# Kernel optimization log

Measured on AMD Instinct MI355X. Metric: run time of the kernel, lower is better.

The kernel has to match this reference:

```python
import jax, jax.numpy as jnp
import numpy as np

L = 3          # layers
D = 256        # hidden_dim
H = 4          # heads
F = 1024       # ffn_size
IMG = (64, 32) # img_dim
S = IMG[0] * IMG[1]
DK = D // H    # key/query head dim
V = 2 * D      # double_v_dim value dim
DV = V // H    # value head dim
B = 2


def _rel_pos():
    # rotary angles, repeated pairwise as in get_rel_pos
    angle = 1.0 / (10000.0 ** jnp.linspace(0.0, 1.0, DK // 2))
    angle = jnp.repeat(angle, 2)                                  # [DK]
    idx = jnp.arange(S, dtype=jnp.float32)
    sin = jnp.sin(idx[:, None] * angle[None, :])                  # [S, DK]
    cos = jnp.cos(idx[:, None] * angle[None, :])
    # per-head causal decay mask, row-normalized by sqrt(rowsum)
    decay = jnp.log(1.0 - 2.0 ** (-5.0 - jnp.arange(H, dtype=jnp.float32)))  # [H]
    diff = idx[:, None] - idx[None, :]                            # [S, S]
    mask = jnp.where(diff >= 0, jnp.exp(diff[None, :, :] * decay[:, None, None]), 0.0)
    mask = mask / jnp.sqrt(mask.sum(-1, keepdims=True))           # [H, S, S]
    return sin, cos, mask


def _theta_shift(x, sin, cos):
    # x: [B, H, S, DK]; rotate-every-two rotary embedding
    x1, x2 = x[..., ::2], x[..., 1::2]
    rot = jnp.stack([-x2, x1], axis=-1).reshape(x.shape)
    return x * cos + rot * sin


def _ln(x, w, b, eps=1e-5):
    mu = x.mean(-1, keepdims=True)
    var = ((x - mu) ** 2).mean(-1, keepdims=True)
    return (x - mu) / jnp.sqrt(var + eps) * w + b


def _retention(x, sin, cos, mask, Wq, Wk, Wv, Wg, Wo):
    b, s, _ = x.shape
    q = (x @ Wq).reshape(b, s, H, DK).transpose(0, 2, 1, 3)
    k = (x @ Wk).reshape(b, s, H, DK).transpose(0, 2, 1, 3) * (DK ** -0.5)
    v = (x @ Wv).reshape(b, s, H, DV).transpose(0, 2, 1, 3)
    g = x @ Wg                                                    # [b, s, V]
    qr = _theta_shift(q, sin, cos)
    kr = _theta_shift(k, sin, cos)
    qk = jnp.einsum('bhsd,bhtd->bhst', qr, kr) * mask[None]
    denom = jnp.clip(jnp.abs(qk).sum(-1, keepdims=True), 1.0, None)
    qk = qk / jax.lax.stop_gradient(denom)
    o = jnp.einsum('bhst,bhtv->bhsv', qk, v)                      # [b, H, s, DV]
    o = o * jax.lax.rsqrt((o ** 2).mean(-1, keepdims=True) + 1e-6)  # per-head RMSNorm
    o = o.transpose(0, 2, 1, 3).reshape(b, s, V)
    o = (g * jax.nn.sigmoid(g)) * o                               # swish gate
    return o @ Wo


def setup_inputs():
    key = jax.random.key(0)
    ks = jax.random.split(key, 16)
    sc = 0.02
    return {
        'x': jax.random.normal(ks[0], (B, S, D), jnp.float32),
        'Wq': jax.random.normal(ks[1], (L, D, D), jnp.float32) * sc,
        'Wk': jax.random.normal(ks[2], (L, D, D), jnp.float32) * sc,
        'Wv': jax.random.normal(ks[3], (L, D, V), jnp.float32) * sc,
        'Wg': jax.random.normal(ks[4], (L, D, V), jnp.float32) * sc,
        'Wo': jax.random.normal(ks[5], (L, V, D), jnp.float32) * sc,
        'ln1_w': jnp.ones((L, D), jnp.float32),
        'ln1_b': jnp.zeros((L, D), jnp.float32),
        'ln2_w': jnp.ones((L, D), jnp.float32),
        'ln2_b': jnp.zeros((L, D), jnp.float32),
        'W1': jax.random.normal(ks[6], (L, D, F), jnp.float32) * sc,
        'b1': jnp.zeros((L, F), jnp.float32),
        'W2': jax.random.normal(ks[7], (L, F, D), jnp.float32) * sc,
        'b2': jnp.zeros((L, D), jnp.float32),
    }


def reference(x, Wq, Wk, Wv, Wg, Wo, ln1_w, ln1_b, ln2_w, ln2_b, W1, b1, W2, b2):
    sin, cos, mask = _rel_pos()
    for i in range(L):
        y = _retention(_ln(x, ln1_w[i], ln1_b[i]), sin, cos, mask,
                       Wq[i], Wk[i], Wv[i], Wg[i], Wo[i]) + x
        h = _ln(y, ln2_w[i], ln2_b[i])
        x = (jax.nn.gelu(h @ W1[i] + b1[i], approximate=False) @ W2[i] + b2[i]) + y
    return x.reshape(x.shape[0], IMG[0], IMG[1], D)
```

## Files before the change

kernel.cpp:

```cpp
#include <hip/hip_runtime.h>
#include <hip/hip_bf16.h>
#include <cstddef>
#include <cmath>
#include <algorithm>

#define SEQ 2048
#define DMODEL 256
#define NHEAD 4
#define DK 64
#define VDIM 512
#define DV 128
#define NB 2
#define FDIM 1024
#define NROWS (NB*SEQ)
#define QKVGN 1536
#define NSLOT 288

typedef unsigned short u16;
typedef __attribute__((ext_vector_type(8))) short short8;
typedef __attribute__((ext_vector_type(4))) short short4v;
typedef __attribute__((ext_vector_type(4))) float f32x4;

static __device__ __forceinline__ u16 f2b(float f) {
    union { float f; unsigned u; } c; c.f = f;
    unsigned r = c.u + 0x7fffu + ((c.u >> 16) & 1u);
    return (u16)(r >> 16);
}
static __device__ __forceinline__ float b2f(u16 u) {
    union { unsigned u; float f; } c; c.u = ((unsigned)u) << 16; return c.f;
}

static __device__ __forceinline__ f32x4 mfma16_bf16(short4v a, short4v b, f32x4 c) {
    return __builtin_amdgcn_mfma_f32_16x16x16bf16_1k(a, b, c, 0, 0, 0);
}

static __device__ __forceinline__ short4v pack_bf16x4(float a0, float a1, float a2, float a3) {
    union { short4v v; unsigned u[2]; } z;
    union { __hip_bfloat162 h; unsigned u; } p0, p1;
    p0.h = __float22bfloat162_rn(make_float2(a0, a1));
    p1.h = __float22bfloat162_rn(make_float2(a2, a3));
    z.u[0] = p0.u; z.u[1] = p1.u;
    return z.v;
}

#define GLOAD_LDS16(GP, LP) \
    __builtin_amdgcn_global_load_lds((const __attribute__((address_space(1))) void*)(GP), \
                                     (__attribute__((address_space(3))) void*)(LP), 16, 0, 0)

__global__ void tables_kernel(float* __restrict__ sint, float* __restrict__ cost)
{
    int idx = blockIdx.x * 256 + threadIdx.x;
    if (idx >= SEQ * DK) return;
    int s = idx >> 6, d = idx & 63;
    int j = d >> 1;
    float a = powf(10000.f, -(float)j / 31.f);
    float arg = (float)s * a;
    sint[idx] = sinf(arg);
    cost[idx] = cosf(arg);
}

__global__ __launch_bounds__(256) void wconv_kernel(const float* __restrict__ in,
                                                    u16* __restrict__ out, int K, int N,
                                                    size_t in_lstride, size_t out_lstride)
{
    __shared__ float tile[32][33];
    int n0 = blockIdx.x * 32, k0 = blockIdx.y * 32;
    const float* inz = in + (size_t)blockIdx.z * in_lstride;
    u16* outz = out + (size_t)blockIdx.z * out_lstride;
    int tx = threadIdx.x, ty = threadIdx.y;
    #pragma unroll
    for (int r = 0; r < 4; ++r) {
        int kr = ty + r * 8;
        tile[kr][tx] = inz[(size_t)(k0 + kr) * N + n0 + tx];
    }
    __syncthreads();
    #pragma unroll
    for (int r = 0; r < 4; ++r) {
        int nr = ty + r * 8;
        outz[(size_t)(n0 + nr) * K + k0 + tx] = f2b(tile[tx][nr]);
    }
}

__global__ __launch_bounds__(256) void ln_kernel(const float* __restrict__ x,
                                                 const float* __restrict__ w,
                                                 const float* __restrict__ b,
                                                 u16* __restrict__ o)
{
    int row = blockIdx.x;
    int t = threadIdx.x;
    float v = x[(size_t)row * DMODEL + t];
    __shared__ float red[256];
    red[t] = v; __syncthreads();
    for (int st = 128; st > 0; st >>= 1) { if (t < st) red[t] += red[t + st]; __syncthreads(); }
    float mu = red[0] * (1.f / DMODEL);
    __syncthreads();
    red[t] = v * v; __syncthreads();
    for (int st = 128; st > 0; st >>= 1) { if (t < st) red[t] += red[t + st]; __syncthreads(); }
    float var = red[0] * (1.f / DMODEL) - mu * mu;
    o[(size_t)row * DMODEL + t] = f2b((v - mu) * rsqrtf(var + 1e-5f) * w[t] + b[t]);
}

template<int NPART, int HASBIAS>
__global__ __launch_bounds__(256) void lncomb_kernel(const u16* __restrict__ pW,
                                                     const float* __restrict__ bias,
                                                     const float* __restrict__ res,
                                                     const float* __restrict__ w,
                                                     const float* __restrict__ b,
                                                     float* __restrict__ yout,
                                                     u16* __restrict__ o)
{
    int row = blockIdx.x;
    int t = threadIdx.x;
    size_t i = (size_t)row * DMODEL + t;
    const size_t PS = (size_t)NROWS * DMODEL;
    float v = res[i];
    #pragma unroll
    for (int k = 0; k < NPART; ++k) v += b2f(pW[i + k * PS]);
    if (HASBIAS) v += bias[t];
    yout[i] = v;
    __shared__ float red[256];
    red[t] = v; __syncthreads();
    for (int st = 128; st > 0; st >>= 1) { if (t < st) red[t] += red[t + st]; __syncthreads(); }
    float mu = red[0] * (1.f / DMODEL);
    __syncthreads();
    red[t] = v * v; __syncthreads();
    for (int st = 128; st > 0; st >>= 1) { if (t < st) red[t] += red[t + st]; __syncthreads(); }
    float var = red[0] * (1.f / DMODEL) - mu * mu;
    o[i] = f2b((v - mu) * rsqrtf(var + 1e-5f) * w[t] + b[t]);
}

__global__ __launch_bounds__(256) void comb4_kernel(const u16* __restrict__ pW,
                                                    const float* __restrict__ bias,
                                                    const float* __restrict__ yb,
                                                    float* __restrict__ out)
{
    int row = blockIdx.x;
    int t = threadIdx.x;
    size_t i = (size_t)row * DMODEL + t;
    const size_t PS = (size_t)NROWS * DMODEL;
    out[i] = b2f(pW[i]) + b2f(pW[i + PS]) + b2f(pW[i + 2 * PS]) + b2f(pW[i + 3 * PS]) + bias[t] + yb[i];
}

template<int BIAS, int GELU, int ROT, int OUTBF, int SPLIT, int VT>
__global__ __launch_bounds__(256) void gemm64(const u16* __restrict__ A,
                                              const u16* __restrict__ Bt,
                                              void* __restrict__ Cout,
                                              const float* __restrict__ bias,
                                              const float* __restrict__ sint,
                                              const float* __restrict__ cost,
                                              u16* __restrict__ vtout,
                                              int M, int N, int K, int kslice)
{
    __shared__ __align__(16) u16 As[2][64 * 64];
    __shared__ __align__(16) u16 Bs[2][64 * 64];
    int bx = blockIdx.x, by = blockIdx.y;
    int tid = threadIdx.x;
    int wave = tid >> 6, lane = tid & 63;
    int wm = wave & 1, wn = wave >> 1;
    int l15 = lane & 15, lg = lane >> 4;
    int kb0 = SPLIT ? blockIdx.z * kslice : 0;
    int kcnt = SPLIT ? kslice : K;

    int L0 = wave * 64 + lane;
    int r0 = L0 >> 3, c0g = (L0 & 7) ^ ((r0 >> 1) & 7);
    int L1 = 256 + wave * 64 + lane;
    int r1 = L1 >> 3, c1g = (L1 & 7) ^ ((r1 >> 1) & 7);
    const u16* Ag0 = A + (size_t)(by * 64 + r0) * K + kb0 + c0g * 8;
    const u16* Ag1 = A + (size_t)(by * 64 + r1) * K + kb0 + c1g * 8;
    const u16* Bg0 = Bt + (size_t)(bx * 64 + r0) * K + kb0 + c0g * 8;
    const u16* Bg1 = Bt + (size_t)(bx * 64 + r1) * K + kb0 + c1g * 8;

#define GSTAGE(BUF, KOFF) do { \
    GLOAD_LDS16(Ag0 + (KOFF), &As[BUF][wave * 512]); \
    GLOAD_LDS16(Ag1 + (KOFF), &As[BUF][2048 + wave * 512]); \
    GLOAD_LDS16(Bg0 + (KOFF), &Bs[BUF][wave * 512]); \
    GLOAD_LDS16(Bg1 + (KOFF), &Bs[BUF][2048 + wave * 512]); \
} while (0)

    f32x4 acc[2][2] = {};
    GSTAGE(0, 0);
    __syncthreads();
    int cur = 0;
    for (int k0 = 0; k0 < kcnt; k0 += 64, cur ^= 1) {
        if (k0 + 64 < kcnt) GSTAGE(cur ^ 1, k0 + 64);
        #pragma unroll
        for (int kk = 0; kk < 2; ++kk) {
            short8 af[2], bf[2];
            #pragma unroll
            for (int i = 0; i < 2; ++i) {
                int ra = wm * 32 + i * 16 + l15;
                int rb = wn * 32 + i * 16 + l15;
                af[i] = *(const short8*)&As[cur][ra * 64 + ((kk * 4 + lg) ^ ((ra >> 1) & 7)) * 8];
                bf[i] = *(const short8*)&Bs[cur][rb * 64 + ((kk * 4 + lg) ^ ((rb >> 1) & 7)) * 8];
            }
            #pragma unroll
            for (int mi = 0; mi < 2; ++mi)
                #pragma unroll
                for (int ni = 0; ni < 2; ++ni)
                    acc[mi][ni] = __builtin_amdgcn_mfma_f32_16x16x32_bf16(af[mi], bf[ni], acc[mi][ni], 0, 0, 0);
        }
        __syncthreads();
    }
#undef GSTAGE

    float* Cf = (float*)Cout;
    u16* Ch = (u16*)Cout;
    u16* Chs = (u16*)Cout;
    #pragma unroll
    for (int mi = 0; mi < 2; ++mi)
        #pragma unroll
        for (int ni = 0; ni < 2; ++ni) {
            int colb = bx * 64 + wn * 32 + ni * 16;
            if (VT && colb >= 512 && colb < 1024) {
                int col = colb + l15;
                int z = ((by >> 5) << 2) + ((col - 512) >> 7);
                int dv = (col - 512) & 127;
                int s0b = (by * 64 + wm * 32) & (SEQ - 1);
                short4v pk = pack_bf16x4(acc[mi][ni][0], acc[mi][ni][1], acc[mi][ni][2], acc[mi][ni][3]);
                *(short4v*)(vtout + (size_t)(z * DV + dv) * SEQ + s0b + lg * 8 + mi * 4) = pk;
            } else {
                #pragma unroll
                for (int r = 0; r < 4; ++r) {
                    int row = by * 64 + wm * 32 + mi * 16 + lg * 4 + r;
                    int col = colb + l15;
                    float v = acc[mi][ni][r];
                    if (ROT) {
                        float pv = __shfl_xor(v, 1);
                        if (col < 512) {
                            int s = row & (SEQ - 1);
                            int dk = col & 63;
                            float c = cost[(s << 6) + dk], sn = sint[(s << 6) + dk];
                            float rv = (col & 1) ? (v * c + pv * sn) : (v * c - pv * sn);
                            v = (col < 256) ? rv : rv * 0.125f;
                        }
                    }
                    if (BIAS) v += bias[col];
                    if (GELU) v = 0.5f * v * (1.f + erff(v * 0.70710678118654752f));
                    if (SPLIT)      Chs[(size_t)blockIdx.z * M * N + (size_t)row * N + col] = f2b(v);
                    else if (OUTBF) Ch[(size_t)row * N + col] = f2b(v);
                    else            Cf[(size_t)row * N + col] = v;
                }
            }
        }
}

__global__ __launch_bounds__(256) void retention_p1(
    const u16* __restrict__ qkvg, const u16* __restrict__ vt,
    u16* __restrict__ po, float* __restrict__ pden)
{
    __shared__ __align__(16) u16 Klds[2][2048];
    __shared__ __align__(16) u16 Vlds[2][4096];

    int bid = blockIdx.x;
    int bh = bid & 7;
    int f = bid >> 3;
    int a = 0, base = 0;
    while (f >= base + 8 * (a + 1)) { base += 8 * (a + 1); ++a; }
    int segs = f - base;
    int qt = 8 * a + segs / (a + 1);
    int ch = segs % (a + 1);
    int b = bh >> 2, h = bh & 3;
    int slot = bh * NSLOT + f;

    int tid = threadIdx.x;
    int wave = tid >> 6, lane = tid & 63;
    int wq = wave >> 1, wv = wave & 1;
    int l15 = lane & 15, lg = lane >> 4;

    float rgeo = 1.f - exp2f(-5.f - (float)h);
    float dec2 = log2f(rgeo);
    float step = exp2f(dec2 * -32.f);

    const u16* qbase  = qkvg + (size_t)b * SEQ * QKVGN + h * 64;
    const u16* kbase  = qbase + 256;
    const u16* vtg    = vt + (size_t)bh * DV * SEQ;

    int q0w = qt * 32 + wq * 16;
    short8 qf0 = *(const short8*)(qbase + (size_t)(q0w + l15) * QKVGN + lg * 8);
    short8 qf1 = *(const short8*)(qbase + (size_t)(q0w + l15) * QKVGN + 32 + lg * 8);

    int tb = ch * 8;
    int t_last = (ch == a) ? qt : (tb + 7);
    int hasdiag = (ch == a);

    float rinv  = exp2f(-dec2);
    float r16   = exp2f(dec2 * -16.f);
    float et00 = exp2f(dec2 * -(float)(tb * 32 + lg * 4));
    float et01 = et00 * rinv;
    float et02 = et01 * rinv;
    float et03 = et02 * rinv;
    float et10 = et00 * r16, et11 = et01 * r16, et12 = et02 * r16, et13 = et03 * r16;

    f32x4 oacc0 = {0.f,0.f,0.f,0.f}, oacc1 = {0.f,0.f,0.f,0.f};
    f32x4 oacc2 = {0.f,0.f,0.f,0.f}, oacc3 = {0.f,0.f,0.f,0.f};
    float den_l = 0.f;

#define STAGE(BUF, TI) do { \
    int t0_ = (TI) * 32; \
    _Pragma("unroll") \
    for (int ii = 0; ii < 3; ++ii) { \
        int inst_ = wave * 3 + ii; \
        if (inst_ < 4) { \
            const u16* g_ = kbase + (size_t)(t0_ + (lane & 31)) * QKVGN + (2 * inst_ + (lane >> 5)) * 8; \
            GLOAD_LDS16(g_, &Klds[BUF][inst_ * 512]); \
        } else { \
            int j_ = inst_ - 4; \
            const u16* g_ = vtg + (size_t)(j_ * 16 + (lane >> 2)) * SEQ + t0_ + (lane & 3) * 8; \
            GLOAD_LDS16(g_, &Vlds[BUF][j_ * 512]); \
        } \
    } \
} while (0)

#define BODY(BUF, DIAG) do { \
    const u16* kb_ = &Klds[BUF][0]; \
    const u16* vb_ = &Vlds[BUF][0]; \
    short8 k00 = *(const short8*)(kb_ + (lg    ) * 256 + l15 * 8); \
    short8 k01 = *(const short8*)(kb_ + (4 + lg) * 256 + l15 * 8); \
    short8 k10 = *(const short8*)(kb_ + (lg    ) * 256 + (16 + l15) * 8); \
    short8 k11 = *(const short8*)(kb_ + (4 + lg) * 256 + (16 + l15) * 8); \
    short8 V0 = *(const short8*)(vb_ + (wv * 64 +      l15) * 32 + lg * 8); \
    short8 V1 = *(const short8*)(vb_ + (wv * 64 + 16 + l15) * 32 + lg * 8); \
    short8 V2 = *(const short8*)(vb_ + (wv * 64 + 32 + l15) * 32 + lg * 8); \
    short8 V3 = *(const short8*)(vb_ + (wv * 64 + 48 + l15) * 32 + lg * 8); \
    f32x4 s0 = {0.f,0.f,0.f,0.f}, s1 = {0.f,0.f,0.f,0.f}; \
    s0 = __builtin_amdgcn_mfma_f32_16x16x32_bf16(k00, qf0, s0, 0, 0, 0); \
    s0 = __builtin_amdgcn_mfma_f32_16x16x32_bf16(k01, qf1, s0, 0, 0, 0); \
    s1 = __builtin_amdgcn_mfma_f32_16x16x32_bf16(k10, qf0, s1, 0, 0, 0); \
    s1 = __builtin_amdgcn_mfma_f32_16x16x32_bf16(k11, qf1, s1, 0, 0, 0); \
    float a0 = s0[0] * et00, a1 = s0[1] * et01, a2 = s0[2] * et02, a3 = s0[3] * et03; \
    float c0 = s1[0] * et10, c1 = s1[1] * et11, c2 = s1[2] * et12, c3 = s1[3] * et13; \
    if (DIAG) { \
        int qr_ = wq * 16 + l15, t0r_ = lg * 4; \
        a0 = (t0r_ +  0 <= qr_) ? a0 : 0.f;  a1 = (t0r_ +  1 <= qr_) ? a1 : 0.f; \
        a2 = (t0r_ +  2 <= qr_) ? a2 : 0.f;  a3 = (t0r_ +  3 <= qr_) ? a3 : 0.f; \
        c0 = (t0r_ + 16 <= qr_) ? c0 : 0.f;  c1 = (t0r_ + 17 <= qr_) ? c1 : 0.f; \
        c2 = (t0r_ + 18 <= qr_) ? c2 : 0.f;  c3 = (t0r_ + 19 <= qr_) ? c3 : 0.f; \
    } \
    den_l += fabsf(a0) + fabsf(a1) + fabsf(a2) + fabsf(a3) \
           + fabsf(c0) + fabsf(c1) + fabsf(c2) + fabsf(c3); \
    short4v pa0 = pack_bf16x4(a0, a1, a2, a3); \
    short4v pa1 = pack_bf16x4(c0, c1, c2, c3); \
    oacc0 = mfma16_bf16(pa0, __builtin_shufflevector(V0, V0, 0, 1, 2, 3), oacc0); \
    oacc1 = mfma16_bf16(pa0, __builtin_shufflevector(V1, V1, 0, 1, 2, 3), oacc1); \
    oacc2 = mfma16_bf16(pa0, __builtin_shufflevector(V2, V2, 0, 1, 2, 3), oacc2); \
    oacc3 = mfma16_bf16(pa0, __builtin_shufflevector(V3, V3, 0, 1, 2, 3), oacc3); \
    oacc0 = mfma16_bf16(pa1, __builtin_shufflevector(V0, V0, 4, 5, 6, 7), oacc0); \
    oacc1 = mfma16_bf16(pa1, __builtin_shufflevector(V1, V1, 4, 5, 6, 7), oacc1); \
    oacc2 = mfma16_bf16(pa1, __builtin_shufflevector(V2, V2, 4, 5, 6, 7), oacc2); \
    oacc3 = mfma16_bf16(pa1, __builtin_shufflevector(V3, V3, 4, 5, 6, 7), oacc3); \
    et00 *= step; et01 *= step; et02 *= step; et03 *= step; \
    et10 *= step; et11 *= step; et12 *= step; et13 *= step; \
} while (0)

    int ti = tb;
    STAGE(0, tb);
    __syncthreads();
    for (; ti + 2 <= t_last; ti += 2) {
        STAGE(1, ti + 1);
        BODY(0, 0);
        __syncthreads();
        STAGE(0, ti + 2);
        BODY(1, 0);
        __syncthreads();
    }
    if (ti < t_last) {
        STAGE(1, ti + 1);
        BODY(0, 0);
        __syncthreads();
        BODY(1, hasdiag);
    } else {
        BODY(0, hasdiag);
    }
#undef STAGE
#undef BODY

    den_l += __shfl_xor(den_l, 16);
    den_l += __shfl_xor(den_l, 32);
    if (lane < 16)
        pden[(size_t)slot * 32 + wq * 16 + l15] = den_l;

    u16* pobase = po + (size_t)slot * (32 * 128) + (wq * 16 + lg * 4) * 128 + wv * 64 + l15;
    #pragma unroll
    for (int r = 0; r < 4; ++r) {
        pobase[r * 128 +  0] = f2b(oacc0[r]);
        pobase[r * 128 + 16] = f2b(oacc1[r]);
        pobase[r * 128 + 32] = f2b(oacc2[r]);
        pobase[r * 128 + 48] = f2b(oacc3[r]);
    }
}

__global__ __launch_bounds__(256) void retention_p2(
    const u16* __restrict__ po, const float* __restrict__ pden,
    const u16* __restrict__ qkvg, u16* __restrict__ og)
{
    int bid = blockIdx.x;
    int bh = bid & 7;
    int qt = bid >> 3;
    int b = bh >> 2, h = bh & 3;
    int aa = qt >> 3;
    int sbase = bh * NSLOT + 4 * aa * (aa + 1) + (qt & 7) * (aa + 1);
    int nch = aa + 1;
    int t = threadIdx.x;
    int row = t >> 3, c0 = (t & 7) * 16;
    int q = qt * 32 + row;

    float den = 0.f;
    for (int k = 0; k < nch; ++k) den += pden[(size_t)(sbase + k) * 32 + row];
    float acc[16];
    #pragma unroll
    for (int j = 0; j < 16; ++j) acc[j] = 0.f;
    for (int k = 0; k < nch; ++k) {
        const u16* p = po + (size_t)(sbase + k) * (32 * 128) + row * 128 + c0;
        #pragma unroll
        for (int j = 0; j < 16; ++j) acc[j] += b2f(p[j]);
    }
    float rgeo = 1.f - exp2f(-5.f - (float)h);
    float dec2 = log2f(rgeo);
    float rp1 = exp2f(dec2 * (float)(q + 1));
    float cs = (1.f - rp1) / (1.f - rgeo);
    float invs = rsqrtf(cs);
    float eqv = exp2f(dec2 * (float)q);
    float d = fmaxf(den * eqv * invs, 1.f);
    float scl = eqv * invs / d;
    float ss = 0.f;
    #pragma unroll
    for (int j = 0; j < 16; ++j) { float v = acc[j] * scl; acc[j] = v; ss += v * v; }
    ss += __shfl_xor(ss, 1); ss += __shfl_xor(ss, 2); ss += __shfl_xor(ss, 4);
    float rms = rsqrtf(ss * (1.f / DV) + 1e-6f);

    const u16* gbase = qkvg + ((size_t)(b * SEQ + q)) * QKVGN + 1024 + h * DV + c0;
    u16* obase = og + ((size_t)(b * SEQ + q)) * VDIM + h * DV + c0;
    #pragma unroll
    for (int j = 0; j < 16; ++j) {
        float gv = b2f(gbase[j]);
        float sig = 1.f / (1.f + __expf(-gv));
        obase[j] = f2b(gv * sig * acc[j] * rms);
    }
}

extern "C" void kernel_launch(void* const* d_in, const int* in_sizes, int n_in,
                              void* d_out, int out_size, void* d_ws, size_t ws_size,
                              hipStream_t stream)
{
    const float* x0    = (const float*)d_in[0];
    const float* Wq    = (const float*)d_in[1];
    const float* Wk    = (const float*)d_in[2];
    const float* Wv    = (const float*)d_in[3];
    const float* Wg    = (const float*)d_in[4];
    const float* Wo    = (const float*)d_in[5];
    const float* ln1w  = (const float*)d_in[6];
    const float* ln1b  = (const float*)d_in[7];
    const float* ln2w  = (const float*)d_in[8];
    const float* ln2b  = (const float*)d_in[9];
    const float* W1    = (const float*)d_in[10];
    const float* b1    = (const float*)d_in[11];
    const float* W2    = (const float*)d_in[12];
    const float* b2    = (const float*)d_in[13];

    char* ws = (char*)d_ws;
    size_t off = 0;
    auto alloc = [&](size_t bytes) { char* p = ws + off; off += (bytes + 255) & ~(size_t)255; return p; };

    float* sin_t = (float*)alloc(SEQ * DK * 4);
    float* cos_t = (float*)alloc(SEQ * DK * 4);
    u16* wqkvg_t = (u16*)alloc((size_t)3 * QKVGN * DMODEL * 2);
    u16* wo_t    = (u16*)alloc((size_t)3 * DMODEL * VDIM * 2);
    u16* w1_t    = (u16*)alloc((size_t)3 * FDIM * DMODEL * 2);
    u16* w2_t    = (u16*)alloc((size_t)3 * DMODEL * FDIM * 2);
    u16* qkvg    = (u16*)alloc((size_t)NROWS * QKVGN * 2);
    u16* xln     = (u16*)alloc((size_t)NROWS * DMODEL * 2);
    u16* vt      = (u16*)alloc((size_t)NB * NHEAD * DV * SEQ * 2);
    float* yb    = (float*)alloc((size_t)NROWS * DMODEL * 4);
    float* xbuf  = (float*)alloc((size_t)NROWS * DMODEL * 4);
    u16* po      = (u16*)alloc((size_t)8 * NSLOT * 32 * 128 * 2);
    float* pden  = (float*)alloc((size_t)8 * NSLOT * 32 * 4);
    u16* ff1 = qkvg;
    u16* h2  = xln;
    u16* ogb = vt;
    u16* pWh = po;

    tables_kernel<<<(SEQ * DK + 255) / 256, 256, 0, stream>>>(sin_t, cos_t);
    dim3 tb(32, 8);
    const size_t WLQ = (size_t)QKVGN * DMODEL;
    wconv_kernel<<<dim3(8, 8, 3),  tb, 0, stream>>>(Wq, wqkvg_t,              DMODEL, DMODEL, (size_t)DMODEL*DMODEL, WLQ);
    wconv_kernel<<<dim3(8, 8, 3),  tb, 0, stream>>>(Wk, wqkvg_t + 256 * 256,  DMODEL, DMODEL, (size_t)DMODEL*DMODEL, WLQ);
    wconv_kernel<<<dim3(16, 8, 3), tb, 0, stream>>>(Wv, wqkvg_t + 512 * 256,  DMODEL, VDIM,   (size_t)DMODEL*VDIM,   WLQ);
    wconv_kernel<<<dim3(16, 8, 3), tb, 0, stream>>>(Wg, wqkvg_t + 1024 * 256, DMODEL, VDIM,   (size_t)DMODEL*VDIM,   WLQ);
    wconv_kernel<<<dim3(8, 16, 3), tb, 0, stream>>>(Wo, wo_t, VDIM,   DMODEL, (size_t)VDIM*DMODEL,   (size_t)VDIM*DMODEL);
    wconv_kernel<<<dim3(32, 8, 3), tb, 0, stream>>>(W1, w1_t, DMODEL, FDIM,   (size_t)DMODEL*FDIM,   (size_t)DMODEL*FDIM);
    wconv_kernel<<<dim3(8, 32, 3), tb, 0, stream>>>(W2, w2_t, FDIM,   DMODEL, (size_t)FDIM*DMODEL,   (size_t)FDIM*DMODEL);

    ln_kernel<<<NROWS, 256, 0, stream>>>(x0, ln1w, ln1b, xln);

    const float* xres = x0;
    for (int i = 0; i < 3; ++i) {
        const u16* wqkvgi = wqkvg_t + (size_t)i * QKVGN * DMODEL;
        const u16* woi = wo_t + (size_t)i * DMODEL * VDIM;
        const u16* w1i = w1_t + (size_t)i * FDIM * DMODEL;
        const u16* w2i = w2_t + (size_t)i * DMODEL * FDIM;

        gemm64<0,0,1,1,0,1><<<dim3(QKVGN/64, NROWS/64), 256, 0, stream>>>(
            xln, wqkvgi, qkvg, nullptr, sin_t, cos_t, vt, NROWS, QKVGN, DMODEL, 0);

        retention_p1<<<dim3(NSLOT * NB * NHEAD), 256, 0, stream>>>(qkvg, vt, po, pden);
        retention_p2<<<dim3((SEQ/32) * NB * NHEAD), 256, 0, stream>>>(po, pden, qkvg, ogb);

        gemm64<0,0,0,0,1,0><<<dim3(DMODEL/64, NROWS/64, 4), 256, 0, stream>>>(
            ogb, woi, pWh, nullptr, nullptr, nullptr, nullptr, NROWS, DMODEL, VDIM, 128);
        lncomb_kernel<4,0><<<NROWS, 256, 0, stream>>>(pWh, nullptr, xres,
            ln2w + i * DMODEL, ln2b + i * DMODEL, yb, h2);

        gemm64<1,1,0,1,0,0><<<dim3(FDIM/64, NROWS/64), 256, 0, stream>>>(
            h2, w1i, ff1, b1 + (size_t)i * FDIM, nullptr, nullptr, nullptr, NROWS, FDIM, DMODEL, 0);

        gemm64<0,0,0,0,1,0><<<dim3(DMODEL/64, NROWS/64, 4), 256, 0, stream>>>(
            ff1, w2i, pWh, nullptr, nullptr, nullptr, nullptr, NROWS, DMODEL, FDIM, 256);

        if (i < 2) {
            lncomb_kernel<4,1><<<NROWS, 256, 0, stream>>>(pWh, b2 + (size_t)i * DMODEL, yb,
                ln1w + (i + 1) * DMODEL, ln1b + (i + 1) * DMODEL, xbuf, xln);
            xres = xbuf;
        } else {
            comb4_kernel<<<NROWS, 256, 0, stream>>>(pWh, b2 + (size_t)i * DMODEL, yb, (float*)d_out);
        }
    }
}
```

Baseline: 282.7 us.

## Fuse split-K reduction, residual add and LayerNorm into following GEMM prologue

Removes the standalone LayerNorm and combine kernels by having the QKVG and FFN1 GEMMs load the full 64x256 A tile themselves. Each block sums the split-K partials, bias and residual, applies LayerNorm, and writes the bf16 result into swizzled LDS before the K loop. Block column 0 also writes the fp32 residual out for later use. This saves several launches and the round trip of the normalized activations through global memory. In exchange, every column block recomputes the LayerNorm for its rows, which adds redundant reads of the partials and residual, and the larger LDS footprint may lower occupancy.

```diff
diff --git a/kernel.cpp b/kernel.cpp
--- a/kernel.cpp
+++ b/kernel.cpp
@@ -43,6 +43,16 @@
     return z.v;
 }
 
+static __device__ __forceinline__ short8 pack_bf16x8(f32x4 a, f32x4 b) {
+    union { short8 v; unsigned u[4]; } z;
+    union { __hip_bfloat162 h; unsigned u; } p;
+    p.h = __float22bfloat162_rn(make_float2(a[0], a[1])); z.u[0] = p.u;
+    p.h = __float22bfloat162_rn(make_float2(a[2], a[3])); z.u[1] = p.u;
+    p.h = __float22bfloat162_rn(make_float2(b[0], b[1])); z.u[2] = p.u;
+    p.h = __float22bfloat162_rn(make_float2(b[2], b[3])); z.u[3] = p.u;
+    return z.v;
+}
+
 #define GLOAD_LDS16(GP, LP) \
     __builtin_amdgcn_global_load_lds((const __attribute__((address_space(1))) void*)(GP), \
                                      (__attribute__((address_space(3))) void*)(LP), 16, 0, 0)
@@ -81,54 +91,6 @@
     }
 }
 
-__global__ __launch_bounds__(256) void ln_kernel(const float* __restrict__ x,
-                                                 const float* __restrict__ w,
-                                                 const float* __restrict__ b,
-                                                 u16* __restrict__ o)
-{
-    int row = blockIdx.x;
-    int t = threadIdx.x;
-    float v = x[(size_t)row * DMODEL + t];
-    __shared__ float red[256];
-    red[t] = v; __syncthreads();
-    for (int st = 128; st > 0; st >>= 1) { if (t < st) red[t] += red[t + st]; __syncthreads(); }
-    float mu = red[0] * (1.f / DMODEL);
-    __syncthreads();
-    red[t] = v * v; __syncthreads();
-    for (int st = 128; st > 0; st >>= 1) { if (t < st) red[t] += red[t + st]; __syncthreads(); }
-    float var = red[0] * (1.f / DMODEL) - mu * mu;
-    o[(size_t)row * DMODEL + t] = f2b((v - mu) * rsqrtf(var + 1e-5f) * w[t] + b[t]);
-}
-
-template<int NPART, int HASBIAS>
-__global__ __launch_bounds__(256) void lncomb_kernel(const u16* __restrict__ pW,
-                                                     const float* __restrict__ bias,
-                                                     const float* __restrict__ res,
-                                                     const float* __restrict__ w,
-                                                     const float* __restrict__ b,
-                                                     float* __restrict__ yout,
-                                                     u16* __restrict__ o)
-{
-    int row = blockIdx.x;
-    int t = threadIdx.x;
-    size_t i = (size_t)row * DMODEL + t;
-    const size_t PS = (size_t)NROWS * DMODEL;
-    float v = res[i];
-    #pragma unroll
-    for (int k = 0; k < NPART; ++k) v += b2f(pW[i + k * PS]);
-    if (HASBIAS) v += bias[t];
-    yout[i] = v;
-    __shared__ float red[256];
-    red[t] = v; __syncthreads();
-    for (int st = 128; st > 0; st >>= 1) { if (t < st) red[t] += red[t + st]; __syncthreads(); }
-    float mu = red[0] * (1.f / DMODEL);
-    __syncthreads();
-    red[t] = v * v; __syncthreads();
-    for (int st = 128; st > 0; st >>= 1) { if (t < st) red[t] += red[t + st]; __syncthreads(); }
-    float var = red[0] * (1.f / DMODEL) - mu * mu;
-    o[i] = f2b((v - mu) * rsqrtf(var + 1e-5f) * w[t] + b[t]);
-}
-
 __global__ __launch_bounds__(256) void comb4_kernel(const u16* __restrict__ pW,
                                                     const float* __restrict__ bias,
                                                     const float* __restrict__ yb,
@@ -141,15 +103,10 @@
     out[i] = b2f(pW[i]) + b2f(pW[i + PS]) + b2f(pW[i + 2 * PS]) + b2f(pW[i + 3 * PS]) + bias[t] + yb[i];
 }
 
-template<int BIAS, int GELU, int ROT, int OUTBF, int SPLIT, int VT>
-__global__ __launch_bounds__(256) void gemm64(const u16* __restrict__ A,
-                                              const u16* __restrict__ Bt,
-                                              void* __restrict__ Cout,
-                                              const float* __restrict__ bias,
-                                              const float* __restrict__ sint,
-                                              const float* __restrict__ cost,
-                                              u16* __restrict__ vtout,
-                                              int M, int N, int K, int kslice)
+__global__ __launch_bounds__(256) void gemm64s(const u16* __restrict__ A,
+                                               const u16* __restrict__ Bt,
+                                               u16* __restrict__ Cout,
+                                               int M, int N, int K, int kslice)
 {
     __shared__ __align__(16) u16 As[2][64 * 64];
     __shared__ __align__(16) u16 Bs[2][64 * 64];
@@ -158,8 +115,7 @@
     int wave = tid >> 6, lane = tid & 63;
     int wm = wave & 1, wn = wave >> 1;
     int l15 = lane & 15, lg = lane >> 4;
-    int kb0 = SPLIT ? blockIdx.z * kslice : 0;
-    int kcnt = SPLIT ? kslice : K;
+    int kb0 = blockIdx.z * kslice;
 
     int L0 = wave * 64 + lane;
     int r0 = L0 >> 3, c0g = (L0 & 7) ^ ((r0 >> 1) & 7);
@@ -181,8 +137,8 @@
     GSTAGE(0, 0);
     __syncthreads();
     int cur = 0;
-    for (int k0 = 0; k0 < kcnt; k0 += 64, cur ^= 1) {
-        if (k0 + 64 < kcnt) GSTAGE(cur ^ 1, k0 + 64);
+    for (int k0 = 0; k0 < kslice; k0 += 64, cur ^= 1) {
+        if (k0 + 64 < kslice) GSTAGE(cur ^ 1, k0 + 64);
         #pragma unroll
         for (int kk = 0; kk < 2; ++kk) {
             short8 af[2], bf[2];
@@ -203,9 +159,134 @@
     }
 #undef GSTAGE
 
-    float* Cf = (float*)Cout;
-    u16* Ch = (u16*)Cout;
-    u16* Chs = (u16*)Cout;
+    u16* Chs = Cout + (size_t)blockIdx.z * M * N;
+    #pragma unroll
+    for (int mi = 0; mi < 2; ++mi)
+        #pragma unroll
+        for (int ni = 0; ni < 2; ++ni)
+            #pragma unroll
+            for (int r = 0; r < 4; ++r) {
+                int row = by * 64 + wm * 32 + mi * 16 + lg * 4 + r;
+                int col = bx * 64 + wn * 32 + ni * 16 + l15;
+                Chs[(size_t)row * N + col] = f2b(acc[mi][ni][r]);
+            }
+}
+
+template<int NPART, int CBIAS, int ROT, int GB, int VT>
+__global__ __launch_bounds__(256) void gemm64f(const u16* __restrict__ pW,
+                                               const float* __restrict__ cbias,
+                                               const float* __restrict__ res,
+                                               const float* __restrict__ lnw,
+                                               const float* __restrict__ lnb,
+                                               float* __restrict__ ycomb,
+                                               const u16* __restrict__ Bt,
+                                               u16* __restrict__ Cout,
+                                               const float* __restrict__ gbias,
+                                               const float* __restrict__ sint,
+                                               const float* __restrict__ cost,
+                                               u16* __restrict__ vtout,
+                                               int N)
+{
+    __shared__ __align__(16) u16 As[64 * 256];
+    __shared__ __align__(16) u16 Bs[2][64 * 64];
+    int bx = blockIdx.x, by = blockIdx.y;
+    int tid = threadIdx.x;
+    int wave = tid >> 6, lane = tid & 63;
+    int wm = wave & 1, wn = wave >> 1;
+    int l15 = lane & 15, lg = lane >> 4;
+    const size_t PS = (size_t)NROWS * DMODEL;
+
+    int L0 = wave * 64 + lane;
+    int r0 = L0 >> 3, c0g = (L0 & 7) ^ ((r0 >> 1) & 7);
+    int L1 = 256 + wave * 64 + lane;
+    int r1 = L1 >> 3, c1g = (L1 & 7) ^ ((r1 >> 1) & 7);
+    const u16* Bg0 = Bt + (size_t)(bx * 64 + r0) * 256 + c0g * 8;
+    const u16* Bg1 = Bt + (size_t)(bx * 64 + r1) * 256 + c1g * 8;
+#define GSTAGEB(BUF, KOFF) do { \
+    GLOAD_LDS16(Bg0 + (KOFF), &Bs[BUF][wave * 512]); \
+    GLOAD_LDS16(Bg1 + (KOFF), &Bs[BUF][2048 + wave * 512]); \
+} while (0)
+
+    GSTAGEB(0, 0);
+
+    {
+        int row = tid >> 2, qu = tid & 3;
+        size_t grow = (size_t)(by * 64 + row);
+        f32x4 v[16];
+        const float* rp = res + grow * 256 + qu * 64;
+        #pragma unroll
+        for (int j = 0; j < 16; ++j) v[j] = *(const f32x4*)(rp + j * 4);
+        #pragma unroll
+        for (int p = 0; p < NPART; ++p) {
+            const u16* pp = pW + (size_t)p * PS + grow * 256 + qu * 64;
+            #pragma unroll
+            for (int j = 0; j < 8; ++j) {
+                short8 sv = *(const short8*)(pp + j * 8);
+                v[2*j][0]   += b2f((u16)sv[0]); v[2*j][1]   += b2f((u16)sv[1]);
+                v[2*j][2]   += b2f((u16)sv[2]); v[2*j][3]   += b2f((u16)sv[3]);
+                v[2*j+1][0] += b2f((u16)sv[4]); v[2*j+1][1] += b2f((u16)sv[5]);
+                v[2*j+1][2] += b2f((u16)sv[6]); v[2*j+1][3] += b2f((u16)sv[7]);
+            }
+        }
+        if (CBIAS) {
+            #pragma unroll
+            for (int j = 0; j < 16; ++j) v[j] += *(const f32x4*)(cbias + qu * 64 + j * 4);
+        }
+        if (NPART > 0 && bx == 0) {
+            float* yp = ycomb + grow * 256 + qu * 64;
+            #pragma unroll
+            for (int j = 0; j < 16; ++j) *(f32x4*)(yp + j * 4) = v[j];
+        }
+        float s = 0.f, s2 = 0.f;
+        #pragma unroll
+        for (int j = 0; j < 16; ++j) {
+            s  += v[j][0] + v[j][1] + v[j][2] + v[j][3];
+            s2 += v[j][0]*v[j][0] + v[j][1]*v[j][1] + v[j][2]*v[j][2] + v[j][3]*v[j][3];
+        }
+        s  += __shfl_xor(s, 1);  s  += __shfl_xor(s, 2);
+        s2 += __shfl_xor(s2, 1); s2 += __shfl_xor(s2, 2);
+        float mu = s * (1.f / 256.f);
+        float var = s2 * (1.f / 256.f) - mu * mu;
+        float rstd = rsqrtf(var + 1e-5f);
+        #pragma unroll
+        for (int j = 0; j < 16; ++j) {
+            f32x4 wv = *(const f32x4*)(lnw + qu * 64 + j * 4);
+            f32x4 bv = *(const f32x4*)(lnb + qu * 64 + j * 4);
+            v[j] = (v[j] - mu) * rstd * wv + bv;
+        }
+        int swb = (row >> 1) & 7;
+        #pragma unroll
+        for (int j2 = 0; j2 < 8; ++j2) {
+            short8 pk = pack_bf16x8(v[2*j2], v[2*j2+1]);
+            *(short8*)&As[row * 256 + (qu * 8 + (j2 ^ swb)) * 8] = pk;
+        }
+    }
+    __syncthreads();
+
+    f32x4 acc[2][2] = {};
+    int cur = 0;
+    for (int k0 = 0; k0 < 256; k0 += 64, cur ^= 1) {
+        if (k0 + 64 < 256) GSTAGEB(cur ^ 1, k0 + 64);
+        #pragma unroll
+        for (int kk = 0; kk < 2; ++kk) {
+            short8 af[2], bf[2];
+            #pragma unroll
+            for (int i = 0; i < 2; ++i) {
+                int ra = wm * 32 + i * 16 + l15;
+                int rb = wn * 32 + i * 16 + l15;
+                af[i] = *(const short8*)&As[ra * 256 + ((k0 >> 3) + ((kk * 4 + lg) ^ ((ra >> 1) & 7))) * 8];
+                bf[i] = *(const short8*)&Bs[cur][rb * 64 + ((kk * 4 + lg) ^ ((rb >> 1) & 7)) * 8];
+            }
+            #pragma unroll
+            for (int mi = 0; mi < 2; ++mi)
+                #pragma unroll
+                for (int ni = 0; ni < 2; ++ni)
+                    acc[mi][ni] = __builtin_amdgcn_mfma_f32_16x16x32_bf16(af[mi], bf[ni], acc[mi][ni], 0, 0, 0);
+        }
+        __syncthreads();
+    }
+#undef GSTAGEB
+
     #pragma unroll
     for (int mi = 0; mi < 2; ++mi)
         #pragma unroll
@@ -234,11 +315,11 @@
                             v = (col < 256) ? rv : rv * 0.125f;
                         }
                     }
-                    if (BIAS) v += bias[col];
-                    if (GELU) v = 0.5f * v * (1.f + erff(v * 0.70710678118654752f));
-                    if (SPLIT)      Chs[(size_t)blockIdx.z * M * N + (size_t)row * N + col] = f2b(v);
-                    else if (OUTBF) Ch[(size_t)row * N + col] = f2b(v);
-                    else            Cf[(size_t)row * N + col] = v;
+                    if (GB) {
+                        v += gbias[col];
+                        v = 0.5f * v * (1.f + erff(v * 0.70710678118654752f));
+                    }
+                    Cout[(size_t)row * N + col] = f2b(v);
                 }
             }
         }
@@ -468,14 +549,12 @@
     u16* w1_t    = (u16*)alloc((size_t)3 * FDIM * DMODEL * 2);
     u16* w2_t    = (u16*)alloc((size_t)3 * DMODEL * FDIM * 2);
     u16* qkvg    = (u16*)alloc((size_t)NROWS * QKVGN * 2);
-    u16* xln     = (u16*)alloc((size_t)NROWS * DMODEL * 2);
     u16* vt      = (u16*)alloc((size_t)NB * NHEAD * DV * SEQ * 2);
     float* yb    = (float*)alloc((size_t)NROWS * DMODEL * 4);
     float* xbuf  = (float*)alloc((size_t)NROWS * DMODEL * 4);
     u16* po      = (u16*)alloc((size_t)8 * NSLOT * 32 * 128 * 2);
     float* pden  = (float*)alloc((size_t)8 * NSLOT * 32 * 4);
     u16* ff1 = qkvg;
-    u16* h2  = xln;
     u16* ogb = vt;
     u16* pWh = po;
 
@@ -490,8 +569,6 @@
     wconv_kernel<<<dim3(32, 8, 3), tb, 0, stream>>>(W1, w1_t, DMODEL, FDIM,   (size_t)DMODEL*FDIM,   (size_t)DMODEL*FDIM);
     wconv_kernel<<<dim3(8, 32, 3), tb, 0, stream>>>(W2, w2_t, FDIM,   DMODEL, (size_t)FDIM*DMODEL,   (size_t)FDIM*DMODEL);
 
-    ln_kernel<<<NROWS, 256, 0, stream>>>(x0, ln1w, ln1b, xln);
-
     const float* xres = x0;
     for (int i = 0; i < 3; ++i) {
         const u16* wqkvgi = wqkvg_t + (size_t)i * QKVGN * DMODEL;
@@ -499,29 +576,30 @@
         const u16* w1i = w1_t + (size_t)i * FDIM * DMODEL;
         const u16* w2i = w2_t + (size_t)i * DMODEL * FDIM;
 
-        gemm64<0,0,1,1,0,1><<<dim3(QKVGN/64, NROWS/64), 256, 0, stream>>>(
-            xln, wqkvgi, qkvg, nullptr, sin_t, cos_t, vt, NROWS, QKVGN, DMODEL, 0);
+        if (i == 0) {
+            gemm64f<0,0,1,0,1><<<dim3(QKVGN/64, NROWS/64), 256, 0, stream>>>(
+                nullptr, nullptr, x0, ln1w, ln1b, nullptr,
+                wqkvgi, qkvg, nullptr, sin_t, cos_t, vt, QKVGN);
+        } else {
+            gemm64f<4,1,1,0,1><<<dim3(QKVGN/64, NROWS/64), 256, 0, stream>>>(
+                pWh, b2 + (size_t)(i - 1) * DMODEL, yb,
+                ln1w + i * DMODEL, ln1b + i * DMODEL, xbuf,
+                wqkvgi, qkvg, nullptr, sin_t, cos_t, vt, QKVGN);
+            xres = xbuf;
+        }
 
         retention_p1<<<dim3(NSLOT * NB * NHEAD), 256, 0, stream>>>(qkvg, vt, po, pden);
         retention_p2<<<dim3((SEQ/32) * NB * NHEAD), 256, 0, stream>>>(po, pden, qkvg, ogb);
 
-        gemm64<0,0,0,0,1,0><<<dim3(DMODEL/64, NROWS/64, 4), 256, 0, stream>>>(
-            ogb, woi, pWh, nullptr, nullptr, nullptr, nullptr, NROWS, DMODEL, VDIM, 128);
-        lncomb_kernel<4,0><<<NROWS, 256, 0, stream>>>(pWh, nullptr, xres,
-            ln2w + i * DMODEL, ln2b + i * DMODEL, yb, h2);
-
-        gemm64<1,1,0,1,0,0><<<dim3(FDIM/64, NROWS/64), 256, 0, stream>>>(
-            h2, w1i, ff1, b1 + (size_t)i * FDIM, nullptr, nullptr, nullptr, NROWS, FDIM, DMODEL, 0);
-
-        gemm64<0,0,0,0,1,0><<<dim3(DMODEL/64, NROWS/64, 4), 256, 0, stream>>>(
-            ff1, w2i, pWh, nullptr, nullptr, nullptr, nullptr, NROWS, DMODEL, FDIM, 256);
-
-        if (i < 2) {
-            lncomb_kernel<4,1><<<NROWS, 256, 0, stream>>>(pWh, b2 + (size_t)i * DMODEL, yb,
-                ln1w + (i + 1) * DMODEL, ln1b + (i + 1) * DMODEL, xbuf, xln);
-            xres = xbuf;
-        } else {
-            comb4_kernel<<<NROWS, 256, 0, stream>>>(pWh, b2 + (size_t)i * DMODEL, yb, (float*)d_out);
-        }
-    }
-}
+        gemm64s<<<dim3(DMODEL/64, NROWS/64, 4), 256, 0, stream>>>(
+            ogb, woi, pWh, NROWS, DMODEL, VDIM, 128);
+
+        gemm64f<4,0,0,1,0><<<dim3(FDIM/64, NROWS/64), 256, 0, stream>>>(
+            pWh, nullptr, xres, ln2w + i * DMODEL, ln2b + i * DMODEL, yb,
+            w1i, ff1, b1 + (size_t)i * FDIM, nullptr, nullptr, nullptr, FDIM);
+
+        gemm64s<<<dim3(DMODEL/64, NROWS/64, 4), 256, 0, stream>>>(
+            ff1, w2i, pWh, NROWS, DMODEL, FDIM, 256);
+    }
+    comb4_kernel<<<NROWS, 256, 0, stream>>>(pWh, b2 + (size_t)2 * DMODEL, yb, (float*)d_out);
+}
```

Result: slower. 614.3 us (+117.3%).
